# Optimization experiments

Measured on AMD Instinct MI355X. Metric: run time of the kernel, lower is better.

The kernel has to match this reference:

```python
import jax, jax.numpy as jnp
import numpy as np

LN_EPS = 1e-5   # torch nn.LayerNorm default
EPS = 1e-6      # module eps for denominator clamp


def _layernorm(x, gamma, beta):
    mu = jnp.mean(x, axis=-1, keepdims=True)
    var = jnp.mean(jnp.square(x - mu), axis=-1, keepdims=True)
    return (x - mu) * jax.lax.rsqrt(var + LN_EPS) * gamma + beta


def _l2norm(x):
    # torch F.normalize(dim=-1): x / max(||x||_2, 1e-12)
    n = jnp.sqrt(jnp.sum(jnp.square(x), axis=-1, keepdims=True))
    return x / jnp.maximum(n, 1e-12)


def setup_inputs() -> dict:
    key = jax.random.key(0)
    kq, kk, kv, kp = jax.random.split(key, 4)
    B, H, T, D = 4, 8, 8192, 64
    num_features = 256
    q = jax.random.normal(kq, (B, H, T, D), dtype=jnp.float32)
    k = jax.random.normal(kk, (B, H, T, D), dtype=jnp.float32)
    v = jax.random.normal(kv, (B, H, T, D), dtype=jnp.float32)
    # _create_projection with ortho=True: QR of (D, num_features) reduced -> Q is (D, D)
    g = jax.random.normal(kp, (D, num_features), dtype=jnp.float32)
    Q, _ = jnp.linalg.qr(g, mode='reduced')            # (D, D) since num_features > D
    proj = Q / jnp.maximum(jnp.sqrt(jnp.sum(Q * Q, axis=0, keepdims=True)), 1e-12)
    proj = proj * (D ** -0.25)
    gamma = jnp.ones((D,), dtype=jnp.float32)
    beta = jnp.zeros((D,), dtype=jnp.float32)
    return {"q": q, "k": k, "v": v, "proj": proj, "gamma": gamma, "beta": beta}


def reference(q, k, v, proj, gamma, beta):
    # LayerNorm over head_dim applied to q, k, v (the torch reshapes are a no-op
    # on the math: it is a per-(b,h,t) LayerNorm over the last dim D)
    qn = _layernorm(q, gamma, beta)
    kn = _layernorm(k, gamma, beta)
    vn = _layernorm(v, gamma, beta)
    qn = _l2norm(qn)
    kn = _l2norm(kn)
    # exp feature maps (clamped), scaled by 0.1
    q_proj = jnp.exp(jnp.clip(jnp.einsum('bhtn,nm->bhtm', qn, proj), -15.0, 15.0)) * 0.1
    k_proj = jnp.exp(jnp.clip(jnp.einsum('bhtn,nm->bhtm', kn, proj), -15.0, 15.0)) * 0.1
    # linear-attention accumulation
    kv = jnp.einsum('bhtm,bhtn->bhmn', k_proj, vn) * 0.1          # [B,H,M,D]
    qkv = jnp.einsum('bhtm,bhmn->bhtn', q_proj, kv) * 0.1         # [B,H,T,D]
    denom = jnp.sum(q_proj * k_proj, axis=-1, keepdims=True)      # [B,H,T,1]
    denom = jnp.maximum(denom, EPS)
    out = qkv / denom
    out = _layernorm(out, gamma, beta)                             # final LN over D
    return out  # [B,H,T,D]
```

## Files before the change

kernel.cpp:

```cpp
#include <hip/hip_runtime.h>
#include <stdint.h>

#define T_    8192
#define D_    64
#define BH_   32
#define CH_   16
#define ROWS_ (T_/CH_)
#define ITERS_ (ROWS_/64)
#define TS    72
#define XS    68
#define LN_EPS 1e-5f
#define EPS_   1e-6f

typedef __attribute__((ext_vector_type(8))) short bh8;
typedef __attribute__((ext_vector_type(4))) short bh4;
typedef __attribute__((ext_vector_type(4))) float f32x4;

__device__ __forceinline__ float bf2f(unsigned short u){ return __uint_as_float(((unsigned)u)<<16); }
__device__ __forceinline__ unsigned short f2bf(float f){
  unsigned u = __float_as_uint(f);
  return (unsigned short)((u + 0x7fffu + ((u>>16)&1u)) >> 16);
}
__device__ __forceinline__ void unp8(uint4 a, float* x){
  x[0]=__uint_as_float(a.x<<16); x[1]=__uint_as_float(a.x&0xffff0000u);
  x[2]=__uint_as_float(a.y<<16); x[3]=__uint_as_float(a.y&0xffff0000u);
  x[4]=__uint_as_float(a.z<<16); x[5]=__uint_as_float(a.z&0xffff0000u);
  x[6]=__uint_as_float(a.w<<16); x[7]=__uint_as_float(a.w&0xffff0000u);
}
__device__ __forceinline__ uint4 pk8(const float* x){
  uint4 r;
  r.x = (unsigned)f2bf(x[0]) | ((unsigned)f2bf(x[1])<<16);
  r.y = (unsigned)f2bf(x[2]) | ((unsigned)f2bf(x[3])<<16);
  r.z = (unsigned)f2bf(x[4]) | ((unsigned)f2bf(x[5])<<16);
  r.w = (unsigned)f2bf(x[6]) | ((unsigned)f2bf(x[7])<<16);
  return r;
}
__device__ __forceinline__ bool is_bf16_buf(const void* gamma){
  return ((const uint32_t*)gamma)[0] != 0x3F800000u;
}
template<bool BF>
__device__ __forceinline__ float ldf(const void* p, long long i){
  if (BF) return bf2f(((const unsigned short*)p)[i]);
  else    return ((const float*)p)[i];
}
template<bool BF>
__device__ __forceinline__ void ld8f(const void* p, long long i, float* x){
  if (BF){ uint4 a = *(const uint4*)((const unsigned short*)p + i); unp8(a,x); }
  else {
    const float* f=(const float*)p + i;
    float4 a=*(const float4*)f, b=*(const float4*)(f+4);
    x[0]=a.x;x[1]=a.y;x[2]=a.z;x[3]=a.w; x[4]=b.x;x[5]=b.y;x[6]=b.z;x[7]=b.w;
  }
}
template<bool BF>
__device__ __forceinline__ void ld16f(const void* p, long long i, float* x){
  ld8f<BF>(p, i, x); ld8f<BF>(p, i+8, x+8);
}
template<bool BF>
__device__ __forceinline__ void st16f(void* p, long long i, const float* z){
  if (BF){
    *(uint4*)((unsigned short*)p+i)   = pk8(z);
    *(uint4*)((unsigned short*)p+i+8) = pk8(z+8);
  } else {
    float* f=(float*)p+i;
    *(float4*)(f   ) = make_float4(z[0],z[1],z[2],z[3]);
    *(float4*)(f+4 ) = make_float4(z[4],z[5],z[6],z[7]);
    *(float4*)(f+8 ) = make_float4(z[8],z[9],z[10],z[11]);
    *(float4*)(f+12) = make_float4(z[12],z[13],z[14],z[15]);
  }
}

__device__ __forceinline__ void ln16(float* x, const float* gam, const float* bet, bool l2){
  float s=0.f;
  #pragma unroll
  for(int j=0;j<16;++j) s+=x[j];
  s += __shfl_xor(s,1); s += __shfl_xor(s,2);
  const float mu = s*(1.f/64.f);
  float vs=0.f;
  #pragma unroll
  for(int j=0;j<16;++j){ x[j]-=mu; vs=fmaf(x[j],x[j],vs); }
  vs += __shfl_xor(vs,1); vs += __shfl_xor(vs,2);
  const float rs = rsqrtf(vs*(1.f/64.f)+LN_EPS);
  float ss=0.f;
  #pragma unroll
  for(int j=0;j<16;++j){ x[j]=fmaf(x[j]*rs, gam[j], bet[j]); ss=fmaf(x[j],x[j],ss); }
  if(l2){
    ss += __shfl_xor(ss,1); ss += __shfl_xor(ss,2);
    const float inv = rsqrtf(fmaxf(ss,1e-24f));
    #pragma unroll
    for(int j=0;j<16;++j) x[j]*=inv;
  }
}

template<bool BF>
__global__ __launch_bounds__(256,2)
void kv_kernel(const void* __restrict__ kg, const void* __restrict__ vg,
               const void* __restrict__ projg, const void* __restrict__ gammag,
               const void* __restrict__ betag, float* __restrict__ kvg){
  if (is_bf16_buf(gammag) != BF) return;
  const int tid=threadIdx.x, lane=tid&63, w=tid>>6;
  const int q4=lane>>4, l16=lane&15;
  const int r=lane>>2,  c=lane&3;
  const int bh=blockIdx.x;
  const long long base=(long long)bh*T_*D_;
  const int t0b=blockIdx.y*ROWS_;

  __shared__ __align__(16) short sm_kn[64*TS];
  __shared__ __align__(16) short sm_vt[64*TS];
  __shared__ __align__(16) short sm_kt[64*TS];

  float gamL[16], betL[16];
  #pragma unroll
  for(int j=0;j<16;++j){ gamL[j]=ldf<BF>(gammag,c*16+j); betL[j]=ldf<BF>(betag,c*16+j); }

  for(int e=tid*8; e<D_*D_; e+=256*8){
    int d=e>>6, m=e&63;
    float t8[8]; ld8f<BF>(projg, e, t8);
    *(uint4*)&sm_kn[d*TS+m] = pk8(t8);
  }
  __syncthreads();
  bh8 bP[4][2];
  #pragma unroll
  for(int nt=0;nt<4;++nt)
    #pragma unroll
    for(int ks=0;ks<2;++ks)
      #pragma unroll
      for(int j=0;j<8;++j)
        bP[nt][ks][j] = sm_kn[(ks*32+q4*8+j)*TS + nt*16+l16];
  __syncthreads();

  f32x4 acc2[4];
  #pragma unroll
  for(int nt=0;nt<4;++nt) acc2[nt]=(f32x4){0.f,0.f,0.f,0.f};

  for(int it=0; it<ITERS_; ++it){
    const int tl=16*w;
    const long long gro = base + (long long)(t0b + it*64 + tl + r)*D_ + c*16;

    float x[16];
    ld16f<BF>(kg, gro, x);
    ln16(x, gamL, betL, true);
    *(uint4*)&sm_kn[(tl+r)*TS + c*16    ] = pk8(x);
    *(uint4*)&sm_kn[(tl+r)*TS + c*16 + 8] = pk8(x+8);

    float y[16];
    ld16f<BF>(vg, gro, y);
    ln16(y, gamL, betL, false);
    #pragma unroll
    for(int j=0;j<16;++j) sm_vt[(c*16+j)*TS + tl + r] = (short)f2bf(y[j]);

    f32x4 c1[4];
    #pragma unroll
    for(int nt=0;nt<4;++nt) c1[nt]=(f32x4){0.f,0.f,0.f,0.f};
    #pragma unroll
    for(int ks=0;ks<2;++ks){
      bh8 af = *(const bh8*)&sm_kn[(tl+l16)*TS + ks*32 + q4*8];
      #pragma unroll
      for(int nt=0;nt<4;++nt)
        c1[nt] = __builtin_amdgcn_mfma_f32_16x16x32_bf16(af, bP[nt][ks], c1[nt], 0,0,0);
    }
    #pragma unroll
    for(int nt=0;nt<4;++nt){
      bh4 p;
      #pragma unroll
      for(int reg=0;reg<4;++reg){
        float e = 0.1f*__expf(fminf(fmaxf(c1[nt][reg],-15.f),15.f));
        p[reg] = (short)f2bf(e);
      }
      *(bh4*)&sm_kt[(nt*16+l16)*TS + tl + q4*4] = p;
    }
    __syncthreads();

    #pragma unroll
    for(int ks=0;ks<2;++ks){
      bh8 af = *(const bh8*)&sm_kt[(tl+l16)*TS + ks*32 + q4*8];
      #pragma unroll
      for(int nt=0;nt<4;++nt){
        bh8 bf = *(const bh8*)&sm_vt[(nt*16+l16)*TS + ks*32 + q4*8];
        acc2[nt] = __builtin_amdgcn_mfma_f32_16x16x32_bf16(af, bf, acc2[nt], 0,0,0);
      }
    }
    __syncthreads();
  }

  float* dst = kvg + bh*D_*D_;
  #pragma unroll
  for(int nt=0;nt<4;++nt)
    #pragma unroll
    for(int reg=0;reg<4;++reg)
      atomicAdd(&dst[(16*w + q4*4 + reg)*D_ + nt*16 + l16], acc2[nt][reg]*0.1f);
}

template<bool BF>
__global__ __launch_bounds__(256,2)
void attn_kernel(const void* __restrict__ qg, const void* __restrict__ kg,
                 const void* __restrict__ projg, const void* __restrict__ gammag,
                 const void* __restrict__ betag, const float* __restrict__ kvg,
                 void* __restrict__ outg){
  if (is_bf16_buf(gammag) != BF) return;
  const int tid=threadIdx.x, lane=tid&63, w=tid>>6;
  const int q4=lane>>4, l16=lane&15;
  const int r=lane>>2,  c=lane&3;
  const int bh=blockIdx.x;
  const long long base=(long long)bh*T_*D_;
  const int t0b=blockIdx.y*ROWS_;

  __shared__ __align__(16) short sm_qn[64*TS];
  __shared__ __align__(16) short sm_kn[64*TS];
  __shared__ __align__(16) short sm_qp[64*TS];
  __shared__ __align__(16) float sm_x [64*XS];

  float gamL[16], betL[16];
  #pragma unroll
  for(int j=0;j<16;++j){ gamL[j]=ldf<BF>(gammag,c*16+j); betL[j]=ldf<BF>(betag,c*16+j); }

  for(int e=tid*8; e<D_*D_; e+=256*8){
    int d=e>>6, m=e&63;
    float t8[8]; ld8f<BF>(projg, e, t8);
    *(uint4*)&sm_qn[d*TS+m] = pk8(t8);
  }
  __syncthreads();
  bh8 bP[4][2];
  #pragma unroll
  for(int nt=0;nt<4;++nt)
    #pragma unroll
    for(int ks=0;ks<2;++ks)
      #pragma unroll
      for(int j=0;j<8;++j)
        bP[nt][ks][j] = sm_qn[(ks*32+q4*8+j)*TS + nt*16+l16];
  __syncthreads();

  {
    const float* kvsrc = kvg + bh*D_*D_;
    for(int e=tid; e<D_*D_; e+=256){
      int f=e>>6, d=e&63;
      sm_qn[d*TS+f] = (short)f2bf(kvsrc[e]);
    }
  }
  __syncthreads();
  bh8 bKV[4][2];
  #pragma unroll
  for(int nt=0;nt<4;++nt)
    #pragma unroll
    for(int ks=0;ks<2;++ks)
      #pragma unroll
      for(int j=0;j<8;++j)
        bKV[nt][ks][j] = sm_qn[(nt*16+l16)*TS + ks*32+q4*8+j];
  __syncthreads();

  for(int it=0; it<ITERS_; ++it){
    const int tl=16*w;
    const long long gro = base + (long long)(t0b + it*64 + tl + r)*D_ + c*16;

    float x[16];
    ld16f<BF>(qg, gro, x);
    ln16(x, gamL, betL, true);
    *(uint4*)&sm_qn[(tl+r)*TS + c*16    ] = pk8(x);
    *(uint4*)&sm_qn[(tl+r)*TS + c*16 + 8] = pk8(x+8);
    ld16f<BF>(kg, gro, x);
    ln16(x, gamL, betL, true);
    *(uint4*)&sm_kn[(tl+r)*TS + c*16    ] = pk8(x);
    *(uint4*)&sm_kn[(tl+r)*TS + c*16 + 8] = pk8(x+8);

    f32x4 qp[4], kp[4];
    #pragma unroll
    for(int nt=0;nt<4;++nt) qp[nt]=(f32x4){0.f,0.f,0.f,0.f};
    #pragma unroll
    for(int ks=0;ks<2;++ks){
      bh8 af = *(const bh8*)&sm_qn[(tl+l16)*TS + ks*32 + q4*8];
      #pragma unroll
      for(int nt=0;nt<4;++nt)
        qp[nt] = __builtin_amdgcn_mfma_f32_16x16x32_bf16(af, bP[nt][ks], qp[nt], 0,0,0);
    }
    #pragma unroll
    for(int nt=0;nt<4;++nt)
      #pragma unroll
      for(int reg=0;reg<4;++reg){
        float e = 0.1f*__expf(fminf(fmaxf(qp[nt][reg],-15.f),15.f));
        qp[nt][reg] = e;
        sm_qp[(tl+q4*4+reg)*TS + nt*16+l16] = (short)f2bf(e);
      }

    #pragma unroll
    for(int nt=0;nt<4;++nt) kp[nt]=(f32x4){0.f,0.f,0.f,0.f};
    #pragma unroll
    for(int ks=0;ks<2;++ks){
      bh8 af = *(const bh8*)&sm_kn[(tl+l16)*TS + ks*32 + q4*8];
      #pragma unroll
      for(int nt=0;nt<4;++nt)
        kp[nt] = __builtin_amdgcn_mfma_f32_16x16x32_bf16(af, bP[nt][ks], kp[nt], 0,0,0);
    }
    float sc[4];
    #pragma unroll
    for(int reg=0;reg<4;++reg){
      float dd=0.f;
      #pragma unroll
      for(int nt=0;nt<4;++nt){
        float kv = 0.1f*__expf(fminf(fmaxf(kp[nt][reg],-15.f),15.f));
        dd = fmaf(qp[nt][reg], kv, dd);
      }
      dd += __shfl_xor(dd,1); dd += __shfl_xor(dd,2);
      dd += __shfl_xor(dd,4); dd += __shfl_xor(dd,8);
      sc[reg] = 0.1f / fmaxf(dd, EPS_);
    }

    f32x4 c3[4];
    #pragma unroll
    for(int nt=0;nt<4;++nt) c3[nt]=(f32x4){0.f,0.f,0.f,0.f};
    #pragma unroll
    for(int ks=0;ks<2;++ks){
      bh8 af = *(const bh8*)&sm_qp[(tl+l16)*TS + ks*32 + q4*8];
      #pragma unroll
      for(int nt=0;nt<4;++nt)
        c3[nt] = __builtin_amdgcn_mfma_f32_16x16x32_bf16(af, bKV[nt][ks], c3[nt], 0,0,0);
    }
    #pragma unroll
    for(int nt=0;nt<4;++nt)
      #pragma unroll
      for(int reg=0;reg<4;++reg)
        sm_x[(tl+q4*4+reg)*XS + nt*16+l16] = c3[nt][reg]*sc[reg];

    float z[16];
    #pragma unroll
    for(int j4=0;j4<4;++j4){
      float4 f = *(const float4*)&sm_x[(tl+r)*XS + c*16 + 4*j4];
      z[4*j4+0]=f.x; z[4*j4+1]=f.y; z[4*j4+2]=f.z; z[4*j4+3]=f.w;
    }
    ln16(z, gamL, betL, false);
    st16f<BF>(outg, gro, z);
  }
}

extern "C" void kernel_launch(void* const* d_in, const int* in_sizes, int n_in,
                              void* d_out, int out_size, void* d_ws, size_t ws_size,
                              hipStream_t stream){
  const void* q     = d_in[0];
  const void* k     = d_in[1];
  const void* v     = d_in[2];
  const void* proj  = d_in[3];
  const void* gamma = d_in[4];
  const void* beta  = d_in[5];

  float* kv = (float*)d_ws;
  hipMemsetAsync(kv, 0, (size_t)BH_*D_*D_*sizeof(float), stream);

  dim3 g(BH_, CH_);
  kv_kernel<false>  <<<g, 256, 0, stream>>>(k, v, proj, gamma, beta, kv);
  kv_kernel<true >  <<<g, 256, 0, stream>>>(k, v, proj, gamma, beta, kv);
  attn_kernel<false><<<g, 256, 0, stream>>>(q, k, proj, gamma, beta, kv, d_out);
  attn_kernel<true ><<<g, 256, 0, stream>>>(q, k, proj, gamma, beta, kv, d_out);
}
```

Before: 255.4 us.

## Swizzle LDS layouts, fuse output LayerNorm in registers, merge dtype launches, double grid

Several changes at once. The bf16 and fp32 template launches become one kernel that branches at runtime, removing two empty launches. The time-axis split goes from 16 to 32 chunks, and occupancy bounds rise to 3 blocks. The transposed V and KV tiles in LDS use an XOR swizzle to avoid bank conflicts, and the K and V global loads are issued together for more memory parallelism. The final LayerNorm now runs on MFMA accumulators with cross-lane shuffles, which drops the fp32 LDS staging buffer, but the output becomes scalar strided stores that may coalesce less well. Doubling the chunks also doubles the atomic adds into the KV buffer.

```diff
diff --git a/kernel.cpp b/kernel.cpp
--- a/kernel.cpp
+++ b/kernel.cpp
@@ -4,11 +4,10 @@
 #define T_    8192
 #define D_    64
 #define BH_   32
-#define CH_   16
+#define CH_   32
 #define ROWS_ (T_/CH_)
 #define ITERS_ (ROWS_/64)
 #define TS    72
-#define XS    68
 #define LN_EPS 1e-5f
 #define EPS_   1e-6f
 
@@ -38,6 +37,8 @@
 __device__ __forceinline__ bool is_bf16_buf(const void* gamma){
   return ((const uint32_t*)gamma)[0] != 0x3F800000u;
 }
+__device__ __forceinline__ int vswb(int d){ return (((d&7) ^ ((d>>3)&6)) << 3); }
+
 template<bool BF>
 __device__ __forceinline__ float ldf(const void* p, long long i){
   if (BF) return bf2f(((const unsigned short*)p)[i]);
@@ -56,19 +57,6 @@
 __device__ __forceinline__ void ld16f(const void* p, long long i, float* x){
   ld8f<BF>(p, i, x); ld8f<BF>(p, i+8, x+8);
 }
-template<bool BF>
-__device__ __forceinline__ void st16f(void* p, long long i, const float* z){
-  if (BF){
-    *(uint4*)((unsigned short*)p+i)   = pk8(z);
-    *(uint4*)((unsigned short*)p+i+8) = pk8(z+8);
-  } else {
-    float* f=(float*)p+i;
-    *(float4*)(f   ) = make_float4(z[0],z[1],z[2],z[3]);
-    *(float4*)(f+4 ) = make_float4(z[4],z[5],z[6],z[7]);
-    *(float4*)(f+8 ) = make_float4(z[8],z[9],z[10],z[11]);
-    *(float4*)(f+12) = make_float4(z[12],z[13],z[14],z[15]);
-  }
-}
 
 __device__ __forceinline__ void ln16(float* x, const float* gam, const float* bet, bool l2){
   float s=0.f;
@@ -93,11 +81,10 @@
 }
 
 template<bool BF>
-__global__ __launch_bounds__(256,2)
-void kv_kernel(const void* __restrict__ kg, const void* __restrict__ vg,
+__device__ __forceinline__ void kv_body(const void* __restrict__ kg, const void* __restrict__ vg,
                const void* __restrict__ projg, const void* __restrict__ gammag,
-               const void* __restrict__ betag, float* __restrict__ kvg){
-  if (is_bf16_buf(gammag) != BF) return;
+               const void* __restrict__ betag, float* __restrict__ kvg,
+               short* sm_kn, short* sm_vt, short* sm_kt){
   const int tid=threadIdx.x, lane=tid&63, w=tid>>6;
   const int q4=lane>>4, l16=lane&15;
   const int r=lane>>2,  c=lane&3;
@@ -105,10 +92,6 @@
   const long long base=(long long)bh*T_*D_;
   const int t0b=blockIdx.y*ROWS_;
 
-  __shared__ __align__(16) short sm_kn[64*TS];
-  __shared__ __align__(16) short sm_vt[64*TS];
-  __shared__ __align__(16) short sm_kt[64*TS];
-
   float gamL[16], betL[16];
   #pragma unroll
   for(int j=0;j<16;++j){ gamL[j]=ldf<BF>(gammag,c*16+j); betL[j]=ldf<BF>(betag,c*16+j); }
@@ -137,17 +120,20 @@
     const int tl=16*w;
     const long long gro = base + (long long)(t0b + it*64 + tl + r)*D_ + c*16;
 
-    float x[16];
+    float x[16], y[16];
     ld16f<BF>(kg, gro, x);
+    ld16f<BF>(vg, gro, y);
+
     ln16(x, gamL, betL, true);
     *(uint4*)&sm_kn[(tl+r)*TS + c*16    ] = pk8(x);
     *(uint4*)&sm_kn[(tl+r)*TS + c*16 + 8] = pk8(x+8);
 
-    float y[16];
-    ld16f<BF>(vg, gro, y);
     ln16(y, gamL, betL, false);
     #pragma unroll
-    for(int j=0;j<16;++j) sm_vt[(c*16+j)*TS + tl + r] = (short)f2bf(y[j]);
+    for(int j=0;j<16;++j){
+      const int d=c*16+j;
+      sm_vt[d*TS + ((tl+r) ^ vswb(d))] = (short)f2bf(y[j]);
+    }
 
     f32x4 c1[4];
     #pragma unroll
@@ -176,8 +162,9 @@
       bh8 af = *(const bh8*)&sm_kt[(tl+l16)*TS + ks*32 + q4*8];
       #pragma unroll
       for(int nt=0;nt<4;++nt){
-        bh8 bf = *(const bh8*)&sm_vt[(nt*16+l16)*TS + ks*32 + q4*8];
-        acc2[nt] = __builtin_amdgcn_mfma_f32_16x16x32_bf16(af, bf, acc2[nt], 0,0,0);
+        const int dn = nt*16+l16;
+        bh8 bv = *(const bh8*)&sm_vt[dn*TS + ((ks*32+q4*8) ^ vswb(dn))];
+        acc2[nt] = __builtin_amdgcn_mfma_f32_16x16x32_bf16(af, bv, acc2[nt], 0,0,0);
       }
     }
     __syncthreads();
@@ -192,12 +179,11 @@
 }
 
 template<bool BF>
-__global__ __launch_bounds__(256,2)
-void attn_kernel(const void* __restrict__ qg, const void* __restrict__ kg,
+__device__ __forceinline__ void attn_body(const void* __restrict__ qg, const void* __restrict__ kg,
                  const void* __restrict__ projg, const void* __restrict__ gammag,
                  const void* __restrict__ betag, const float* __restrict__ kvg,
-                 void* __restrict__ outg){
-  if (is_bf16_buf(gammag) != BF) return;
+                 void* __restrict__ outg,
+                 short* sm_qn, short* sm_kn, short* sm_qp){
   const int tid=threadIdx.x, lane=tid&63, w=tid>>6;
   const int q4=lane>>4, l16=lane&15;
   const int r=lane>>2,  c=lane&3;
@@ -205,62 +191,58 @@
   const long long base=(long long)bh*T_*D_;
   const int t0b=blockIdx.y*ROWS_;
 
-  __shared__ __align__(16) short sm_qn[64*TS];
-  __shared__ __align__(16) short sm_kn[64*TS];
-  __shared__ __align__(16) short sm_qp[64*TS];
-  __shared__ __align__(16) float sm_x [64*XS];
-
   float gamL[16], betL[16];
   #pragma unroll
   for(int j=0;j<16;++j){ gamL[j]=ldf<BF>(gammag,c*16+j); betL[j]=ldf<BF>(betag,c*16+j); }
+  float gamF[4], betF[4];
+  #pragma unroll
+  for(int nt=0;nt<4;++nt){ gamF[nt]=ldf<BF>(gammag,nt*16+l16); betF[nt]=ldf<BF>(betag,nt*16+l16); }
 
   for(int e=tid*8; e<D_*D_; e+=256*8){
     int d=e>>6, m=e&63;
     float t8[8]; ld8f<BF>(projg, e, t8);
     *(uint4*)&sm_qn[d*TS+m] = pk8(t8);
   }
-  __syncthreads();
-  bh8 bP[4][2];
-  #pragma unroll
-  for(int nt=0;nt<4;++nt)
-    #pragma unroll
-    for(int ks=0;ks<2;++ks)
-      #pragma unroll
-      for(int j=0;j<8;++j)
-        bP[nt][ks][j] = sm_qn[(ks*32+q4*8+j)*TS + nt*16+l16];
-  __syncthreads();
-
   {
     const float* kvsrc = kvg + bh*D_*D_;
     for(int e=tid; e<D_*D_; e+=256){
       int f=e>>6, d=e&63;
-      sm_qn[d*TS+f] = (short)f2bf(kvsrc[e]);
+      sm_kn[d*TS + (f ^ vswb(d))] = (short)f2bf(kvsrc[e]);
     }
   }
   __syncthreads();
+  bh8 bP[4][2];
+  #pragma unroll
+  for(int nt=0;nt<4;++nt)
+    #pragma unroll
+    for(int ks=0;ks<2;++ks)
+      #pragma unroll
+      for(int j=0;j<8;++j)
+        bP[nt][ks][j] = sm_qn[(ks*32+q4*8+j)*TS + nt*16+l16];
   bh8 bKV[4][2];
   #pragma unroll
   for(int nt=0;nt<4;++nt)
     #pragma unroll
-    for(int ks=0;ks<2;++ks)
-      #pragma unroll
-      for(int j=0;j<8;++j)
-        bKV[nt][ks][j] = sm_qn[(nt*16+l16)*TS + ks*32+q4*8+j];
+    for(int ks=0;ks<2;++ks){
+      const int dn = nt*16+l16;
+      bKV[nt][ks] = *(const bh8*)&sm_kn[dn*TS + ((ks*32+q4*8) ^ vswb(dn))];
+    }
   __syncthreads();
 
   for(int it=0; it<ITERS_; ++it){
     const int tl=16*w;
     const long long gro = base + (long long)(t0b + it*64 + tl + r)*D_ + c*16;
 
-    float x[16];
-    ld16f<BF>(qg, gro, x);
-    ln16(x, gamL, betL, true);
-    *(uint4*)&sm_qn[(tl+r)*TS + c*16    ] = pk8(x);
-    *(uint4*)&sm_qn[(tl+r)*TS + c*16 + 8] = pk8(x+8);
-    ld16f<BF>(kg, gro, x);
-    ln16(x, gamL, betL, true);
-    *(uint4*)&sm_kn[(tl+r)*TS + c*16    ] = pk8(x);
-    *(uint4*)&sm_kn[(tl+r)*TS + c*16 + 8] = pk8(x+8);
+    float xq[16], xk[16];
+    ld16f<BF>(qg, gro, xq);
+    ld16f<BF>(kg, gro, xk);
+
+    ln16(xq, gamL, betL, true);
+    *(uint4*)&sm_qn[(tl+r)*TS + c*16    ] = pk8(xq);
+    *(uint4*)&sm_qn[(tl+r)*TS + c*16 + 8] = pk8(xq+8);
+    ln16(xk, gamL, betL, true);
+    *(uint4*)&sm_kn[(tl+r)*TS + c*16    ] = pk8(xk);
+    *(uint4*)&sm_kn[(tl+r)*TS + c*16 + 8] = pk8(xk+8);
 
     f32x4 qp[4], kp[4];
     #pragma unroll
@@ -314,21 +296,55 @@
       for(int nt=0;nt<4;++nt)
         c3[nt] = __builtin_amdgcn_mfma_f32_16x16x32_bf16(af, bKV[nt][ks], c3[nt], 0,0,0);
     }
-    #pragma unroll
-    for(int nt=0;nt<4;++nt)
-      #pragma unroll
-      for(int reg=0;reg<4;++reg)
-        sm_x[(tl+q4*4+reg)*XS + nt*16+l16] = c3[nt][reg]*sc[reg];
-
-    float z[16];
-    #pragma unroll
-    for(int j4=0;j4<4;++j4){
-      float4 f = *(const float4*)&sm_x[(tl+r)*XS + c*16 + 4*j4];
-      z[4*j4+0]=f.x; z[4*j4+1]=f.y; z[4*j4+2]=f.z; z[4*j4+3]=f.w;
-    }
-    ln16(z, gamL, betL, false);
-    st16f<BF>(outg, gro, z);
-  }
+
+    float rs4[4];
+    #pragma unroll
+    for(int reg=0;reg<4;++reg){
+      float s=0.f;
+      #pragma unroll
+      for(int nt=0;nt<4;++nt){ c3[nt][reg] *= sc[reg]; s += c3[nt][reg]; }
+      s += __shfl_xor(s,1); s += __shfl_xor(s,2); s += __shfl_xor(s,4); s += __shfl_xor(s,8);
+      const float mu = s*(1.f/64.f);
+      float vs=0.f;
+      #pragma unroll
+      for(int nt=0;nt<4;++nt){ const float dd=c3[nt][reg]-mu; c3[nt][reg]=dd; vs=fmaf(dd,dd,vs); }
+      vs += __shfl_xor(vs,1); vs += __shfl_xor(vs,2); vs += __shfl_xor(vs,4); vs += __shfl_xor(vs,8);
+      rs4[reg] = rsqrtf(vs*(1.f/64.f)+LN_EPS);
+    }
+    const long long obase = base + (long long)(t0b + it*64 + tl + q4*4)*D_ + l16;
+    #pragma unroll
+    for(int reg=0;reg<4;++reg)
+      #pragma unroll
+      for(int nt=0;nt<4;++nt){
+        const float z = fmaf(c3[nt][reg]*rs4[reg], gamF[nt], betF[nt]);
+        const long long oi = obase + (long long)reg*D_ + nt*16;
+        if (BF) ((unsigned short*)outg)[oi] = f2bf(z);
+        else    ((float*)outg)[oi]          = z;
+      }
+  }
+}
+
+__global__ __launch_bounds__(256,3)
+void kv_kernel(const void* __restrict__ kg, const void* __restrict__ vg,
+               const void* __restrict__ projg, const void* __restrict__ gammag,
+               const void* __restrict__ betag, float* __restrict__ kvg){
+  __shared__ __align__(16) short sm_kn[64*TS];
+  __shared__ __align__(16) short sm_vt[64*TS];
+  __shared__ __align__(16) short sm_kt[64*TS];
+  if (is_bf16_buf(gammag)) kv_body<true >(kg,vg,projg,gammag,betag,kvg,sm_kn,sm_vt,sm_kt);
+  else                     kv_body<false>(kg,vg,projg,gammag,betag,kvg,sm_kn,sm_vt,sm_kt);
+}
+
+__global__ __launch_bounds__(256,3)
+void attn_kernel(const void* __restrict__ qg, const void* __restrict__ kg,
+                 const void* __restrict__ projg, const void* __restrict__ gammag,
+                 const void* __restrict__ betag, const float* __restrict__ kvg,
+                 void* __restrict__ outg){
+  __shared__ __align__(16) short sm_qn[64*TS];
+  __shared__ __align__(16) short sm_kn[64*TS];
+  __shared__ __align__(16) short sm_qp[64*TS];
+  if (is_bf16_buf(gammag)) attn_body<true >(qg,kg,projg,gammag,betag,kvg,outg,sm_qn,sm_kn,sm_qp);
+  else                     attn_body<false>(qg,kg,projg,gammag,betag,kvg,outg,sm_qn,sm_kn,sm_qp);
 }
 
 extern "C" void kernel_launch(void* const* d_in, const int* in_sizes, int n_in,
@@ -345,8 +361,6 @@
   hipMemsetAsync(kv, 0, (size_t)BH_*D_*D_*sizeof(float), stream);
 
   dim3 g(BH_, CH_);
-  kv_kernel<false>  <<<g, 256, 0, stream>>>(k, v, proj, gamma, beta, kv);
-  kv_kernel<true >  <<<g, 256, 0, stream>>>(k, v, proj, gamma, beta, kv);
-  attn_kernel<false><<<g, 256, 0, stream>>>(q, k, proj, gamma, beta, kv, d_out);
-  attn_kernel<true ><<<g, 256, 0, stream>>>(q, k, proj, gamma, beta, kv, d_out);
-}
+  kv_kernel  <<<g, 256, 0, stream>>>(k, v, proj, gamma, beta, kv);
+  attn_kernel<<<g, 256, 0, stream>>>(q, k, proj, gamma, beta, kv, d_out);
+}
```

After: 308.2 us. 20.7% more time.
